# Kernel tuning notes

Measured on AMD Instinct MI355X. Metric: run time of the kernel, lower is better.

The kernel has to match this reference:

```python
import jax, jax.numpy as jnp
import numpy as np

VOCAB = 32000
DIM = 1024
SEQ = 4096


def setup_inputs() -> dict:
    key = jax.random.key(0)
    ks = jax.random.split(key, 6)
    x = jax.random.randint(ks[0], (1, SEQ), 0, VOCAB, dtype=jnp.int64 if jax.config.jax_enable_x64 else jnp.int32)
    emb = jax.random.normal(ks[1], (VOCAB, DIM), dtype=jnp.float32) * 0.02
    norm_w = jnp.ones((DIM,), dtype=jnp.float32)
    Wq = jax.random.normal(ks[2], (DIM, DIM), dtype=jnp.float32) * (1.0 / np.sqrt(DIM))
    Wk = jax.random.normal(ks[3], (DIM, DIM), dtype=jnp.float32) * (1.0 / np.sqrt(DIM))
    Wv = jax.random.normal(ks[4], (DIM, DIM), dtype=jnp.float32) * (1.0 / np.sqrt(DIM))
    return {"x": x, "emb": emb, "norm_w": norm_w, "Wq": Wq, "Wk": Wk, "Wv": Wv}


def reference(x, emb, norm_w, Wq, Wk, Wv):
    # embedding lookup: [1, S, D]
    h = emb[x]
    # RMSNorm (torch nn.RMSNorm with eps=None -> finfo(dtype).eps)
    eps = jnp.finfo(h.dtype).eps
    h = h * jax.lax.rsqrt(jnp.mean(h * h, axis=-1, keepdims=True) + eps) * norm_w
    h = h[0]  # squeeze(0) -> [S, D]
    # QKV projections (torch Linear: y = x @ W.T)
    q = h @ Wq.T
    k = h @ Wk.T
    v = h @ Wv.T
    # NOTE: faithful to source -- no 1/sqrt(d) scaling, no causal mask
    attn = jax.nn.softmax(q @ k.T, axis=-1)  # [S, S]
    out = attn @ v  # [S, D]
    return jax.nn.silu(out)
```

## Files before the change

kernel.cpp:

```cpp
#include <hip/hip_runtime.h>
#include <stdint.h>

#define SEQ 4096
#define DIM 1024

typedef __bf16 bf16x8 __attribute__((ext_vector_type(8)));
typedef float f32x4 __attribute__((ext_vector_type(4)));
typedef unsigned short u16;

__device__ __forceinline__ u16 f2bf(float f) {
    unsigned u = __float_as_uint(f);
    u += 0x7fffu + ((u >> 16) & 1u);
    return (u16)(u >> 16);
}
__device__ __forceinline__ float bf2f(u16 h) {
    return __uint_as_float(((unsigned)h) << 16);
}

__device__ __forceinline__ void gload16(const u16* g, u16* l) {
    __builtin_amdgcn_global_load_lds(
        (const __attribute__((address_space(1))) void*)g,
        (__attribute__((address_space(3))) void*)l, 16, 0, 0);
}

__global__ __launch_bounds__(256) void embed_rmsnorm_split(
    const int* __restrict__ x, const float* __restrict__ emb,
    const float* __restrict__ nw, u16* __restrict__ hh, u16* __restrict__ hl)
{
    const int row  = blockIdx.x;
    const int t    = threadIdx.x;
    const int lane = t & 63, wave = t >> 6;

    bool i64 = true;
    #pragma unroll
    for (int i = 1; i < 128; i += 2) i64 = i64 && (x[i] == 0);
    const int id = i64 ? x[2 * row] : x[row];

    float4 e = *(const float4*)(emb + (size_t)id * DIM + t * 4);
    float ss = e.x*e.x + e.y*e.y + e.z*e.z + e.w*e.w;
    #pragma unroll
    for (int off = 32; off > 0; off >>= 1) ss += __shfl_down(ss, off);

    __shared__ float red[4];
    if (lane == 0) red[wave] = ss;
    __syncthreads();
    float sum = red[0] + red[1] + red[2] + red[3];
    float scale = rsqrtf(sum * (1.0f / DIM) + 1.1920929e-7f);

    float4 n = *(const float4*)(nw + t * 4);
    float o0 = e.x * scale * n.x;
    float o1 = e.y * scale * n.y;
    float o2 = e.z * scale * n.z;
    float o3 = e.w * scale * n.w;
    ushort4 oh, ol;
    u16 b;
    b = f2bf(o0); oh.x = b; ol.x = f2bf(o0 - bf2f(b));
    b = f2bf(o1); oh.y = b; ol.y = f2bf(o1 - bf2f(b));
    b = f2bf(o2); oh.z = b; ol.z = f2bf(o2 - bf2f(b));
    b = f2bf(o3); oh.w = b; ol.w = f2bf(o3 - bf2f(b));
    *(ushort4*)(hh + (size_t)row * DIM + t * 4) = oh;
    *(ushort4*)(hl + (size_t)row * DIM + t * 4) = ol;
}

__global__ __launch_bounds__(256) void split_w(
    const float* __restrict__ W0, const float* __restrict__ W1,
    const float* __restrict__ W2, u16* __restrict__ H, u16* __restrict__ L)
{
    const float* W = (blockIdx.y == 0) ? W0 : (blockIdx.y == 1) ? W1 : W2;
    const size_t base = (size_t)blockIdx.y * DIM * DIM;
    const int i = (blockIdx.x * 256 + threadIdx.x) * 4;
    float4 w = *(const float4*)(W + i);
    ushort4 h, l;
    u16 b;
    b = f2bf(w.x); h.x = b; l.x = f2bf(w.x - bf2f(b));
    b = f2bf(w.y); h.y = b; l.y = f2bf(w.y - bf2f(b));
    b = f2bf(w.z); h.z = b; l.z = f2bf(w.z - bf2f(b));
    b = f2bf(w.w); h.w = b; l.w = f2bf(w.w - bf2f(b));
    *(ushort4*)(H + base + i) = h;
    *(ushort4*)(L + base + i) = l;
}

__global__ __launch_bounds__(256, 3) void gemm_qkv(
    const u16* __restrict__ Ah, const u16* __restrict__ Al,
    const u16* __restrict__ Bh, const u16* __restrict__ Bl,
    u16* __restrict__ qhl, u16* __restrict__ khl, u16* __restrict__ vT)
{
    __shared__ __align__(16) u16 Ash[128 * 32];
    __shared__ __align__(16) u16 Asl[128 * 32];
    __shared__ __align__(16) u16 Bsh[128 * 32];
    __shared__ __align__(16) u16 Bsl[128 * 32];

    const int tid  = threadIdx.x;
    const int lane = tid & 63;
    const int wave = tid >> 6;
    const int m0   = blockIdx.y * 128;
    const int n0   = blockIdx.x * 128;
    const int wr   = (wave >> 1) * 64;
    const int wc   = (wave & 1) * 64;
    const int half = lane >> 4;
    const int l16  = lane & 15;

    f32x4 acc[4][4] = {};

    const int arow = tid >> 2;
    const int acol = (tid & 3) * 8;
    const int wb   = wave * 512;

    for (int k0 = 0; k0 < DIM; k0 += 32) {
        __syncthreads();
        const size_t aoff = (size_t)(m0 + arow) * DIM + k0 + acol;
        const size_t boff = (size_t)(n0 + arow) * DIM + k0 + acol;
        gload16(Ah + aoff,            &Ash[wb]);
        gload16(Ah + aoff + 64 * DIM, &Ash[2048 + wb]);
        gload16(Al + aoff,            &Asl[wb]);
        gload16(Al + aoff + 64 * DIM, &Asl[2048 + wb]);
        gload16(Bh + boff,            &Bsh[wb]);
        gload16(Bh + boff + 64 * DIM, &Bsh[2048 + wb]);
        gload16(Bl + boff,            &Bsl[wb]);
        gload16(Bl + boff + 64 * DIM, &Bsl[2048 + wb]);
        __syncthreads();

        bf16x8 afh[4], afl[4], bfh[4], bfl[4];
        #pragma unroll
        for (int i = 0; i < 4; ++i) {
            afh[i] = *(const bf16x8*)&Ash[(wr + i*16 + l16) * 32 + half * 8];
            afl[i] = *(const bf16x8*)&Asl[(wr + i*16 + l16) * 32 + half * 8];
        }
        #pragma unroll
        for (int j = 0; j < 4; ++j) {
            bfh[j] = *(const bf16x8*)&Bsh[(wc + j*16 + l16) * 32 + half * 8];
            bfl[j] = *(const bf16x8*)&Bsl[(wc + j*16 + l16) * 32 + half * 8];
        }
        #pragma unroll
        for (int i = 0; i < 4; ++i)
            #pragma unroll
            for (int j = 0; j < 4; ++j) {
                acc[i][j] = __builtin_amdgcn_mfma_f32_16x16x32_bf16(afh[i], bfh[j], acc[i][j], 0, 0, 0);
                acc[i][j] = __builtin_amdgcn_mfma_f32_16x16x32_bf16(afh[i], bfl[j], acc[i][j], 0, 0, 0);
                acc[i][j] = __builtin_amdgcn_mfma_f32_16x16x32_bf16(afl[i], bfh[j], acc[i][j], 0, 0, 0);
            }
    }

    const int reg = n0 >> 10;
    #pragma unroll
    for (int i = 0; i < 4; ++i)
        #pragma unroll
        for (int j = 0; j < 4; ++j)
            #pragma unroll
            for (int r = 0; r < 4; ++r) {
                int row = m0 + wr + i * 16 + half * 4 + r;
                int col = n0 + wc + j * 16 + l16;
                float val = acc[i][j][r];
                u16 hi = f2bf(val);
                if (reg == 0) {
                    qhl[(size_t)row * 2048 + col]        = hi;
                    qhl[(size_t)row * 2048 + col + 1024] = f2bf(val - bf2f(hi));
                } else if (reg == 1) {
                    int c = col - 1024;
                    khl[(size_t)row * 2048 + c]          = hi;
                    khl[(size_t)row * 2048 + c + 1024]   = f2bf(val - bf2f(hi));
                } else {
                    vT[(size_t)(col - 2048) * SEQ + row] = hi;
                }
            }
}

__global__ __launch_bounds__(256, 3) void gemm_sc(
    const u16* __restrict__ Q, const u16* __restrict__ Kk,
    float* __restrict__ C)
{
    __shared__ __align__(16) u16 As[128 * 32];
    __shared__ __align__(16) u16 Bs[128 * 32];

    const int tid  = threadIdx.x;
    const int lane = tid & 63;
    const int wave = tid >> 6;
    const int m0   = blockIdx.y * 128;
    const int n0   = blockIdx.x * 128;
    const int wr   = (wave >> 1) * 64;
    const int wc   = (wave & 1) * 64;
    const int half = lane >> 4;
    const int l16  = lane & 15;

    f32x4 acc[4][4] = {};
    const int arow = tid >> 2;
    const int acol = (tid & 3) * 8;
    const int wb   = wave * 512;

    for (int k0 = 0; k0 < 3072; k0 += 32) {
        const int ka = (k0 < 2048) ? k0 : k0 - 2048;
        const int kb = (k0 < 1024) ? k0 : k0 - 1024;
        __syncthreads();
        gload16(Q  + (size_t)(m0 + arow)      * 2048 + ka + acol, &As[wb]);
        gload16(Q  + (size_t)(m0 + 64 + arow) * 2048 + ka + acol, &As[2048 + wb]);
        gload16(Kk + (size_t)(n0 + arow)      * 2048 + kb + acol, &Bs[wb]);
        gload16(Kk + (size_t)(n0 + 64 + arow) * 2048 + kb + acol, &Bs[2048 + wb]);
        __syncthreads();

        bf16x8 af[4], bfr[4];
        #pragma unroll
        for (int i = 0; i < 4; ++i)
            af[i] = *(const bf16x8*)&As[(wr + i*16 + l16) * 32 + half * 8];
        #pragma unroll
        for (int j = 0; j < 4; ++j)
            bfr[j] = *(const bf16x8*)&Bs[(wc + j*16 + l16) * 32 + half * 8];
        #pragma unroll
        for (int i = 0; i < 4; ++i)
            #pragma unroll
            for (int j = 0; j < 4; ++j)
                acc[i][j] = __builtin_amdgcn_mfma_f32_16x16x32_bf16(af[i], bfr[j], acc[i][j], 0, 0, 0);
    }

    #pragma unroll
    for (int i = 0; i < 4; ++i)
        #pragma unroll
        for (int j = 0; j < 4; ++j)
            #pragma unroll
            for (int r = 0; r < 4; ++r) {
                int row = m0 + wr + i * 16 + half * 4 + r;
                int col = n0 + wc + j * 16 + l16;
                C[(size_t)row * SEQ + col] = acc[i][j][r];
            }
}

__global__ __launch_bounds__(256) void softmax_rows(float* __restrict__ S)
{
    const int row  = blockIdx.x;
    const int t    = threadIdx.x;
    const int lane = t & 63, wave = t >> 6;
    float* rp = S + (size_t)row * SEQ;

    float v[16];
    #pragma unroll
    for (int i = 0; i < 4; ++i) {
        float4 f = *(const float4*)(rp + i * 1024 + t * 4);
        v[i*4+0] = f.x; v[i*4+1] = f.y; v[i*4+2] = f.z; v[i*4+3] = f.w;
    }

    float m = v[0];
    #pragma unroll
    for (int i = 1; i < 16; ++i) m = fmaxf(m, v[i]);
    #pragma unroll
    for (int off = 32; off > 0; off >>= 1) m = fmaxf(m, __shfl_down(m, off));
    __shared__ float red[4];
    if (lane == 0) red[wave] = m;
    __syncthreads();
    m = fmaxf(fmaxf(red[0], red[1]), fmaxf(red[2], red[3]));
    __syncthreads();

    float s = 0.0f;
    #pragma unroll
    for (int i = 0; i < 16; ++i) { v[i] = __expf(v[i] - m); s += v[i]; }
    #pragma unroll
    for (int off = 32; off > 0; off >>= 1) s += __shfl_down(s, off);
    if (lane == 0) red[wave] = s;
    __syncthreads();
    s = red[0] + red[1] + red[2] + red[3];
    float inv = 1.0f / s;

    u16* op = (u16*)rp;
    #pragma unroll
    for (int i = 0; i < 4; ++i) {
        ushort4 o;
        o.x = f2bf(v[i*4+0] * inv);
        o.y = f2bf(v[i*4+1] * inv);
        o.z = f2bf(v[i*4+2] * inv);
        o.w = f2bf(v[i*4+3] * inv);
        *(ushort4*)(op + i * 1024 + t * 4) = o;
    }
}

__global__ __launch_bounds__(256, 3) void gemm_pv_partial(
    const u16* __restrict__ A, const u16* __restrict__ B,
    float* __restrict__ P0, float* __restrict__ P1)
{
    __shared__ __align__(16) u16 As[128 * 32];
    __shared__ __align__(16) u16 Bs[128 * 32];

    const int tid  = threadIdx.x;
    const int lane = tid & 63;
    const int wave = tid >> 6;
    const int m0   = blockIdx.y * 128;
    const int n0   = blockIdx.x * 128;
    const int wr   = (wave >> 1) * 64;
    const int wc   = (wave & 1) * 64;
    const int half = lane >> 4;
    const int l16  = lane & 15;

    float* C = blockIdx.z ? P1 : P0;
    const int kbase = blockIdx.z * 2048;

    f32x4 acc[4][4] = {};
    const int arow = tid >> 2;
    const int acol = (tid & 3) * 8;
    const int wb   = wave * 512;

    for (int k0 = kbase; k0 < kbase + 2048; k0 += 32) {
        __syncthreads();
        gload16(A + (size_t)(m0 + arow)      * 8192 + k0 + acol, &As[wb]);
        gload16(A + (size_t)(m0 + 64 + arow) * 8192 + k0 + acol, &As[2048 + wb]);
        gload16(B + (size_t)(n0 + arow)      * 4096 + k0 + acol, &Bs[wb]);
        gload16(B + (size_t)(n0 + 64 + arow) * 4096 + k0 + acol, &Bs[2048 + wb]);
        __syncthreads();

        bf16x8 af[4], bfr[4];
        #pragma unroll
        for (int i = 0; i < 4; ++i)
            af[i] = *(const bf16x8*)&As[(wr + i*16 + l16) * 32 + half * 8];
        #pragma unroll
        for (int j = 0; j < 4; ++j)
            bfr[j] = *(const bf16x8*)&Bs[(wc + j*16 + l16) * 32 + half * 8];
        #pragma unroll
        for (int i = 0; i < 4; ++i)
            #pragma unroll
            for (int j = 0; j < 4; ++j)
                acc[i][j] = __builtin_amdgcn_mfma_f32_16x16x32_bf16(af[i], bfr[j], acc[i][j], 0, 0, 0);
    }

    #pragma unroll
    for (int i = 0; i < 4; ++i)
        #pragma unroll
        for (int j = 0; j < 4; ++j)
            #pragma unroll
            for (int r = 0; r < 4; ++r) {
                int row = m0 + wr + i * 16 + half * 4 + r;
                int col = n0 + wc + j * 16 + l16;
                C[(size_t)row * DIM + col] = acc[i][j][r];
            }
}

__global__ __launch_bounds__(256) void combine_silu(
    const float* __restrict__ P0, const float* __restrict__ P1,
    float* __restrict__ out)
{
    const int i = (blockIdx.x * 256 + threadIdx.x) * 4;
    float4 a = *(const float4*)(P0 + i);
    float4 b = *(const float4*)(P1 + i);
    float4 o;
    float v;
    v = a.x + b.x; o.x = v / (1.0f + __expf(-v));
    v = a.y + b.y; o.y = v / (1.0f + __expf(-v));
    v = a.z + b.z; o.z = v / (1.0f + __expf(-v));
    v = a.w + b.w; o.w = v / (1.0f + __expf(-v));
    *(float4*)(out + i) = o;
}

extern "C" void kernel_launch(void* const* d_in, const int* in_sizes, int n_in,
                              void* d_out, int out_size, void* d_ws, size_t ws_size,
                              hipStream_t stream)
{
    const int*   x   = (const int*)d_in[0];
    const float* emb = (const float*)d_in[1];
    const float* nw  = (const float*)d_in[2];
    const float* Wq  = (const float*)d_in[3];
    const float* Wk  = (const float*)d_in[4];
    const float* Wv  = (const float*)d_in[5];
    float* out = (float*)d_out;

    char* ws = (char*)d_ws;
    u16*   vT  = (u16*)(ws);
    u16*   qhl = (u16*)(ws + ( 8u << 20));
    u16*   khl = (u16*)(ws + (24u << 20));
    float* Sc  = (float*)(ws + (40u << 20));
    u16*   hh  = (u16*)(ws + (40u << 20));
    u16*   hl  = (u16*)(ws + (48u << 20));
    u16*   Wh  = (u16*)(ws + (56u << 20));
    u16*   Wl  = (u16*)(ws + (62u << 20));
    float* P0  = (float*)(ws + ( 8u << 20));
    float* P1  = (float*)(ws + (24u << 20));

    embed_rmsnorm_split<<<SEQ, 256, 0, stream>>>(x, emb, nw, hh, hl);
    split_w<<<dim3(DIM * DIM / 1024, 3), 256, 0, stream>>>(Wq, Wk, Wv, Wh, Wl);

    gemm_qkv<<<dim3(3072 / 128, SEQ / 128), 256, 0, stream>>>(
        hh, hl, Wh, Wl, qhl, khl, vT);

    gemm_sc<<<dim3(SEQ / 128, SEQ / 128), 256, 0, stream>>>(qhl, khl, Sc);

    softmax_rows<<<SEQ, 256, 0, stream>>>(Sc);

    gemm_pv_partial<<<dim3(DIM / 128, SEQ / 128, 2), 256, 0, stream>>>(
        (const u16*)Sc, vT, P0, P1);

    combine_silu<<<SEQ * DIM / 1024, 256, 0, stream>>>(P0, P1, out);
}
```

Before: 459.4 us.

## Rewrite score GEMM as 256x256 double-buffered 8-wave pipelined kernel

Replaces the 128x128 single-buffered QK^T score GEMM with a 256x256 tile, 512-thread kernel. It uses double-buffered LDS with 64-wide K steps, interleaves global-to-LDS loads across four MFMA phases, raises wave priority during MFMA phases, swizzles the LDS layout to avoid bank conflicts, and swizzles the workgroup order for L2 locality. This targets the global-load stalls and low data reuse of the old synchronous loop. In exchange it needs far more LDS and registers per block, leaving fewer resident blocks, and relies on hand-placed waitcnt and barrier timing that must stay correct.

Result: faster. 444.9 us (-3.2%).

```diff
diff --git a/kernel.cpp b/kernel.cpp
--- a/kernel.cpp
+++ b/kernel.cpp
@@ -165,62 +165,175 @@
             }
 }
 
-__global__ __launch_bounds__(256, 3) void gemm_sc(
+#define SC_NT 48
+__global__ __launch_bounds__(512, 2) void gemm_sc_8ph(
     const u16* __restrict__ Q, const u16* __restrict__ Kk,
     float* __restrict__ C)
 {
-    __shared__ __align__(16) u16 As[128 * 32];
-    __shared__ __align__(16) u16 Bs[128 * 32];
+    __shared__ __align__(16) u16 Alds[2][256 * 64];
+    __shared__ __align__(16) u16 Blds[2][256 * 64];
 
     const int tid  = threadIdx.x;
     const int lane = tid & 63;
-    const int wave = tid >> 6;
-    const int m0   = blockIdx.y * 128;
-    const int n0   = blockIdx.x * 128;
-    const int wr   = (wave >> 1) * 64;
-    const int wc   = (wave & 1) * 64;
+    const int wid  = tid >> 6;
+    const int wm   = wid >> 2;
+    const int wn   = wid & 3;
+    const int l16  = lane & 15;
     const int half = lane >> 4;
-    const int l16  = lane & 15;
-
-    f32x4 acc[4][4] = {};
-    const int arow = tid >> 2;
-    const int acol = (tid & 3) * 8;
-    const int wb   = wave * 512;
-
-    for (int k0 = 0; k0 < 3072; k0 += 32) {
-        const int ka = (k0 < 2048) ? k0 : k0 - 2048;
-        const int kb = (k0 < 1024) ? k0 : k0 - 1024;
-        __syncthreads();
-        gload16(Q  + (size_t)(m0 + arow)      * 2048 + ka + acol, &As[wb]);
-        gload16(Q  + (size_t)(m0 + 64 + arow) * 2048 + ka + acol, &As[2048 + wb]);
-        gload16(Kk + (size_t)(n0 + arow)      * 2048 + kb + acol, &Bs[wb]);
-        gload16(Kk + (size_t)(n0 + 64 + arow) * 2048 + kb + acol, &Bs[2048 + wb]);
-        __syncthreads();
-
-        bf16x8 af[4], bfr[4];
-        #pragma unroll
-        for (int i = 0; i < 4; ++i)
-            af[i] = *(const bf16x8*)&As[(wr + i*16 + l16) * 32 + half * 8];
-        #pragma unroll
-        for (int j = 0; j < 4; ++j)
-            bfr[j] = *(const bf16x8*)&Bs[(wc + j*16 + l16) * 32 + half * 8];
-        #pragma unroll
-        for (int i = 0; i < 4; ++i)
-            #pragma unroll
-            for (int j = 0; j < 4; ++j)
-                acc[i][j] = __builtin_amdgcn_mfma_f32_16x16x32_bf16(af[i], bfr[j], acc[i][j], 0, 0, 0);
-    }
-
-    #pragma unroll
-    for (int i = 0; i < 4; ++i)
-        #pragma unroll
-        for (int j = 0; j < 4; ++j)
-            #pragma unroll
-            for (int r = 0; r < 4; ++r) {
-                int row = m0 + wr + i * 16 + half * 4 + r;
-                int col = n0 + wc + j * 16 + l16;
-                C[(size_t)row * SEQ + col] = acc[i][j][r];
-            }
+
+    const int wg  = blockIdx.y * 16 + blockIdx.x;
+    const int swz = (wg & 7) * 32 + (wg >> 3);
+    const int m0  = (swz >> 4) * 256;
+    const int n0  = (swz & 15) * 256;
+
+    const int tp   = tid ^ (((tid >> 5) & 1) << 1);
+    const int srow = tp >> 3;
+    const int scol = (tp & 7) * 8;
+    const u16* paq[4];
+    const u16* pbq[4];
+    #pragma unroll
+    for (int q = 0; q < 4; ++q) {
+        paq[q] = Q  + (size_t)(m0 + q * 64 + srow) * 2048 + scol;
+        pbq[q] = Kk + (size_t)(n0 + q * 64 + srow) * 2048 + scol;
+    }
+
+    const int s2    = (l16 >> 2) & 1;
+    const int hc    = (half * 8) ^ (s2 << 4);
+    const int abase = (wm * 128 + l16) * 64 + hc;
+    const int bbase = (wn * 64 + l16) * 64 + hc;
+
+    {
+        u16* a0d = &Alds[0][wid * 512];
+        u16* b0d = &Blds[0][wid * 512];
+        u16* a1d = &Alds[1][wid * 512];
+        u16* b1d = &Blds[1][wid * 512];
+        #pragma unroll
+        for (int q = 0; q < 4; ++q) gload16(paq[q],      a0d + q * 4096);
+        #pragma unroll
+        for (int q = 0; q < 4; ++q) gload16(pbq[q],      b0d + q * 4096);
+        #pragma unroll
+        for (int q = 0; q < 4; ++q) gload16(paq[q] + 64, a1d + q * 4096);
+        #pragma unroll
+        for (int q = 0; q < 4; ++q) gload16(pbq[q] + 64, b1d + q * 4096);
+    }
+    asm volatile("s_waitcnt vmcnt(8)" ::: "memory");
+    __builtin_amdgcn_sched_barrier(0);
+    __builtin_amdgcn_s_barrier();
+
+    f32x4 acc[8][4] = {};
+    bf16x8 a0[4][2], b0[2][2], b1[2][2];
+
+    #pragma unroll 1
+    for (int t = 0; t < SC_NT; ++t) {
+        const int  b        = t & 1;
+        const bool do_stage = (t + 2) < SC_NT;
+        const int  k2  = (t + 2) * 64;
+        const int  ka2 = (k2 < 2048) ? k2 : k2 - 2048;
+        const int  kb2 = (k2 < 1024) ? k2 : k2 - 1024;
+        u16* ald = &Alds[b][wid * 512];
+        u16* bld = &Blds[b][wid * 512];
+
+        #pragma unroll
+        for (int i = 0; i < 4; ++i)
+            #pragma unroll
+            for (int ks = 0; ks < 2; ++ks)
+                a0[i][ks] = *(const bf16x8*)&Alds[b][abase + i * 1024 + ks * 32];
+        #pragma unroll
+        for (int g = 0; g < 2; ++g)
+            #pragma unroll
+            for (int ks = 0; ks < 2; ++ks)
+                b0[g][ks] = *(const bf16x8*)&Blds[b][bbase + g * 1024 + ks * 32];
+        __builtin_amdgcn_s_barrier();
+        asm volatile("s_waitcnt lgkmcnt(0)" ::: "memory");
+        __builtin_amdgcn_sched_barrier(0);
+        __builtin_amdgcn_s_setprio(1);
+        #pragma unroll
+        for (int i = 0; i < 4; ++i)
+            #pragma unroll
+            for (int g = 0; g < 2; ++g)
+                #pragma unroll
+                for (int ks = 0; ks < 2; ++ks)
+                    acc[i][g] = __builtin_amdgcn_mfma_f32_16x16x32_bf16(a0[i][ks], b0[g][ks], acc[i][g], 0, 0, 0);
+        __builtin_amdgcn_s_setprio(0);
+        __builtin_amdgcn_s_barrier();
+
+        #pragma unroll
+        for (int g = 0; g < 2; ++g)
+            #pragma unroll
+            for (int ks = 0; ks < 2; ++ks)
+                b1[g][ks] = *(const bf16x8*)&Blds[b][bbase + 2048 + g * 1024 + ks * 32];
+        if (do_stage) {
+            gload16(paq[0] + ka2, ald);
+            gload16(paq[2] + ka2, ald + 2 * 4096);
+        }
+        __builtin_amdgcn_s_barrier();
+        asm volatile("s_waitcnt lgkmcnt(0)" ::: "memory");
+        __builtin_amdgcn_sched_barrier(0);
+        __builtin_amdgcn_s_setprio(1);
+        #pragma unroll
+        for (int i = 0; i < 4; ++i)
+            #pragma unroll
+            for (int g = 0; g < 2; ++g)
+                #pragma unroll
+                for (int ks = 0; ks < 2; ++ks)
+                    acc[i][2 + g] = __builtin_amdgcn_mfma_f32_16x16x32_bf16(a0[i][ks], b1[g][ks], acc[i][2 + g], 0, 0, 0);
+        __builtin_amdgcn_s_setprio(0);
+        __builtin_amdgcn_s_barrier();
+
+        #pragma unroll
+        for (int i = 0; i < 4; ++i)
+            #pragma unroll
+            for (int ks = 0; ks < 2; ++ks)
+                a0[i][ks] = *(const bf16x8*)&Alds[b][abase + 4096 + i * 1024 + ks * 32];
+        if (do_stage) {
+            gload16(pbq[0] + kb2, bld);
+            gload16(pbq[1] + kb2, bld + 4096);
+            gload16(pbq[2] + kb2, bld + 2 * 4096);
+            gload16(pbq[3] + kb2, bld + 3 * 4096);
+        }
+        __builtin_amdgcn_s_barrier();
+        asm volatile("s_waitcnt lgkmcnt(0)" ::: "memory");
+        __builtin_amdgcn_sched_barrier(0);
+        __builtin_amdgcn_s_setprio(1);
+        #pragma unroll
+        for (int i = 0; i < 4; ++i)
+            #pragma unroll
+            for (int g = 0; g < 2; ++g)
+                #pragma unroll
+                for (int ks = 0; ks < 2; ++ks)
+                    acc[4 + i][2 + g] = __builtin_amdgcn_mfma_f32_16x16x32_bf16(a0[i][ks], b1[g][ks], acc[4 + i][2 + g], 0, 0, 0);
+        __builtin_amdgcn_s_setprio(0);
+        __builtin_amdgcn_s_barrier();
+
+        if (do_stage) {
+            gload16(paq[1] + ka2, ald + 4096);
+            gload16(paq[3] + ka2, ald + 3 * 4096);
+        }
+        __builtin_amdgcn_s_barrier();
+        __builtin_amdgcn_s_setprio(1);
+        #pragma unroll
+        for (int i = 0; i < 4; ++i)
+            #pragma unroll
+            for (int g = 0; g < 2; ++g)
+                #pragma unroll
+                for (int ks = 0; ks < 2; ++ks)
+                    acc[4 + i][g] = __builtin_amdgcn_mfma_f32_16x16x32_bf16(a0[i][ks], b0[g][ks], acc[4 + i][g], 0, 0, 0);
+        __builtin_amdgcn_s_setprio(0);
+        if (t < SC_NT - 2) { asm volatile("s_waitcnt vmcnt(8)" ::: "memory"); }
+        else               { asm volatile("s_waitcnt vmcnt(0)" ::: "memory"); }
+        __builtin_amdgcn_sched_barrier(0);
+        __builtin_amdgcn_s_barrier();
+    }
+
+    const int crow0 = m0 + wm * 128 + half * 4;
+    const int ccol0 = n0 + wn * 64 + l16;
+    #pragma unroll
+    for (int mf = 0; mf < 8; ++mf)
+        #pragma unroll
+        for (int nf = 0; nf < 4; ++nf)
+            #pragma unroll
+            for (int r = 0; r < 4; ++r)
+                C[(size_t)(crow0 + mf * 16 + r) * SEQ + ccol0 + nf * 16] = acc[mf][nf][r];
 }
 
 __global__ __launch_bounds__(256) void softmax_rows(float* __restrict__ S)
@@ -375,7 +488,7 @@
     gemm_qkv<<<dim3(3072 / 128, SEQ / 128), 256, 0, stream>>>(
         hh, hl, Wh, Wl, qhl, khl, vT);
 
-    gemm_sc<<<dim3(SEQ / 128, SEQ / 128), 256, 0, stream>>>(qhl, khl, Sc);
+    gemm_sc_8ph<<<dim3(SEQ / 256, SEQ / 256), 512, 0, stream>>>(qhl, khl, Sc);
 
     softmax_rows<<<SEQ, 256, 0, stream>>>(Sc);
 
```
